# Optimization experiments

Measured on AMD Instinct MI355X. Metric: run time of the kernel, lower is better.

## Reference

```python
import jax, jax.numpy as jnp
import numpy as np
from jax import lax

D_MODEL = 1024
STATE_DIM = 512
BATCH = 4
SEQ_LEN = 8192


def _cayley_eigenvalues(a_params, n):
    # a_full = [0, a_1..a_half, -a_half-1..., antisymmetric tail]
    half = n // 2
    a_full = jnp.zeros((n,), dtype=a_params.dtype)
    a_full = a_full.at[1:half + 1].set(a_params)
    a_full = a_full.at[half + 1:].set(-a_params[::-1][: n - half - 1])
    a_hat = jnp.fft.fft(a_full)            # complex64
    omega = jnp.imag(a_hat)                # (n,), float32
    ones = jnp.ones_like(omega)
    num = lax.complex(ones, -omega)
    den = lax.complex(ones, omega)
    return num / den                        # (n,), |lambda|=1


def setup_inputs() -> dict:
    key = jax.random.key(0)
    k1, k2, k3, k4 = jax.random.split(key, 4)
    u = jax.random.normal(k1, (BATCH, SEQ_LEN, D_MODEL), dtype=jnp.float32)
    a_params = jax.random.normal(k2, (STATE_DIM // 2,), dtype=jnp.float32) * 0.1
    # torch Linear weights: B.weight (state_dim, d_model), C.weight (d_model, state_dim)
    B_w = jax.random.normal(k3, (STATE_DIM, D_MODEL), dtype=jnp.float32) / np.sqrt(D_MODEL)
    C_w = jax.random.normal(k4, (D_MODEL, STATE_DIM), dtype=jnp.float32) / np.sqrt(STATE_DIM)
    D = jnp.ones((D_MODEL,), dtype=jnp.float32)
    return {"u": u, "a_params": a_params, "B_w": B_w, "C_w": C_w, "D": D}


def reference(u, a_params, B_w, C_w, D):
    batch, seq_len, d = u.shape
    n = B_w.shape[0]
    # 1) input projection: (b, t, n)
    Bu = jnp.einsum("btd,nd->btn", u, B_w)
    # 2) per-channel geometric kernel k_j[t] = lambda_j^t
    eig = _cayley_eigenvalues(a_params, n)                 # (n,) complex64
    t = jnp.arange(seq_len, dtype=jnp.float32)
    kernel = jnp.exp(t[:, None] * jnp.log(eig)[None, :])   # (T, n) complex64
    # 3) causal convolution via FFT with next-pow2(2T) padding
    fft_len = 1
    while fft_len < 2 * seq_len:
        fft_len *= 2
    pad = fft_len - seq_len
    kernel_padded = jnp.pad(kernel, ((0, pad), (0, 0)))
    K_hat = jnp.fft.fft(kernel_padded, axis=0)             # (F, n)
    Bu_padded = jnp.pad(Bu, ((0, 0), (0, pad), (0, 0))).astype(jnp.complex64)
    Bu_hat = jnp.fft.fft(Bu_padded, axis=1)                # (b, F, n)
    h = jnp.fft.ifft(K_hat[None] * Bu_hat, axis=1).real[:, :seq_len, :]
    # 4) output projection + skip
    y = jnp.einsum("btn,dn->btd", h, C_w) + D * u
    return y
```

## Files before the change

### kernel.cpp

```cpp
#include <hip/hip_runtime.h>
#include <cstdint>
#include <cstddef>

#define D_MODEL   1024
#define STATE_DIM 512
#define BATCH     4
#define SEQ_LEN   8192
#define M_TOTAL   (BATCH * SEQ_LEN)

typedef unsigned short ushort_t;
typedef __attribute__((ext_vector_type(8))) __bf16 bf16x8;
typedef __attribute__((ext_vector_type(4))) float  f32x4;


__device__ inline ushort_t f2bf(float f) {
  union { float f; uint32_t u; } v; v.f = f;
  uint32_t u = v.u;
  uint32_t r = (u + 0x7FFFu + ((u >> 16) & 1u)) >> 16;
  return (ushort_t)r;
}

__device__ inline void llds16(const void* g, void* l) {
  __builtin_amdgcn_global_load_lds(
      (__attribute__((address_space(1))) void*)(void*)g,
      (__attribute__((address_space(3))) void*)l,
      16, 0, 0);
}


__global__ void convert_f32_bf16(const float* __restrict__ in,
                                 ushort_t* __restrict__ out, int n4) {
  int i = blockIdx.x * blockDim.x + threadIdx.x;
  if (i >= n4) return;
  const float4 v = ((const float4*)in)[i];
  ushort4 o;
  o.x = f2bf(v.x); o.y = f2bf(v.y); o.z = f2bf(v.z); o.w = f2bf(v.w);
  ((ushort4*)out)[i] = o;
}


__global__ void eigen_kernel(const float* __restrict__ a_params,
                             float* __restrict__ lam) {
  __shared__ float af[STATE_DIM];
  const int k = threadIdx.x;
  float v = 0.f;
  if (k >= 1 && k <= STATE_DIM / 2)      v = a_params[k - 1];
  else if (k > STATE_DIM / 2)            v = -a_params[STATE_DIM - k];
  af[k] = v;
  __syncthreads();
  float om = 0.f;
  const float c = 6.283185307179586f / 512.0f;
  for (int n = 1; n < STATE_DIM; ++n) {
    int p = (k * n) & 511;
    om -= af[n] * sinf(c * (float)p);
  }
  const float d  = 1.f / (1.f + om * om);
  const float lr = (1.f - om * om) * d;
  const float li = -2.f * om * d;
  double th = atan2((double)li, (double)lr) * 128.0;
  lam[k]        = lr;
  lam[512 + k]  = li;
  lam[1024 + k] = (float)cos(th);
  lam[1536 + k] = (float)sin(th);
}


template <int KDIM, int NDIM, bool FUSE_SKIP>
__global__ __launch_bounds__(256, 2)
void gemm_bt(const ushort_t* __restrict__ A,
             const ushort_t* __restrict__ Bw,
             float* __restrict__ out,
             const float* __restrict__ skip_u,
             const float* __restrict__ Dvec) {
  __shared__ __align__(16) ushort_t smA[128 * 32];
  __shared__ __align__(16) ushort_t smB[128 * 32];
  const int tid    = threadIdx.x;
  const int wave   = tid >> 6, lane = tid & 63;
  const int lane16 = lane & 15, quad = lane >> 4;
  const int wm = (wave & 1) * 64, wn = (wave >> 1) * 64;
  const int row0 = blockIdx.x * 128;
  const int col0 = blockIdx.y * 128;

  f32x4 acc[4][4];
#pragma unroll
  for (int i = 0; i < 4; ++i)
#pragma unroll
    for (int j = 0; j < 4; ++j) {
      f32x4 z = {0.f, 0.f, 0.f, 0.f};
      acc[i][j] = z;
    }

  for (int k0 = 0; k0 < KDIM; k0 += 32) {
#pragma unroll
    for (int s = 0; s < 2; ++s) {
      const int c = s * 256 + tid;
      const ushort_t* gA = A  + (size_t)(row0 + (c >> 2)) * KDIM + k0 + (c & 3) * 8;
      const ushort_t* gB = Bw + (size_t)(col0 + (c >> 2)) * KDIM + k0 + (c & 3) * 8;
      const int ldsoff = (s * 256 + wave * 64) * 16;
      llds16(gA, (char*)smA + ldsoff);
      llds16(gB, (char*)smB + ldsoff);
    }
    __syncthreads();

    bf16x8 af[4], bfr[4];
#pragma unroll
    for (int mi = 0; mi < 4; ++mi)
      af[mi] = *(const bf16x8*)(smA + (wm + mi * 16 + lane16) * 32 + quad * 8);
#pragma unroll
    for (int ni = 0; ni < 4; ++ni)
      bfr[ni] = *(const bf16x8*)(smB + (wn + ni * 16 + lane16) * 32 + quad * 8);
#pragma unroll
    for (int mi = 0; mi < 4; ++mi)
#pragma unroll
      for (int ni = 0; ni < 4; ++ni)
        acc[mi][ni] = __builtin_amdgcn_mfma_f32_16x16x32_bf16(
            af[mi], bfr[ni], acc[mi][ni], 0, 0, 0);
    __syncthreads();
  }

#pragma unroll
  for (int mi = 0; mi < 4; ++mi) {
#pragma unroll
    for (int ni = 0; ni < 4; ++ni) {
      const int row = row0 + wm + mi * 16 + quad * 4;
      const int col = col0 + wn + ni * 16 + lane16;
      float dv = 0.f;
      if (FUSE_SKIP) dv = Dvec[col];
#pragma unroll
      for (int r = 0; r < 4; ++r) {
        const size_t o = (size_t)(row + r) * NDIM + col;
        float val = acc[mi][ni][r];
        if (FUSE_SKIP) val = fmaf(dv, skip_u[o], val);
        out[o] = val;
      }
    }
  }
}


#define NCHUNK 64
#define CLEN   128
#define SOFF   (BATCH * NCHUNK * STATE_DIM)

__global__ __launch_bounds__(512)
void scan_chunks(const float* __restrict__ Bu, const float* __restrict__ lam,
                 float* __restrict__ S) {
  const int j = threadIdx.x;
  const int c = blockIdx.x & (NCHUNK - 1);
  const int b = blockIdx.x >> 6;
  const float lr = lam[j], li = lam[512 + j];
  const float* p = Bu + ((size_t)(b * SEQ_LEN + c * CLEN)) * STATE_DIM + j;
  float hr = 0.f, hi = 0.f;
#pragma unroll 4
  for (int t = 0; t < CLEN; ++t) {
    const float x  = p[(size_t)t * STATE_DIM];
    const float nr = fmaf(lr, hr, fmaf(-li, hi, x));
    const float ni = fmaf(lr, hi, li * hr);
    hr = nr; hi = ni;
  }
  const size_t o = (size_t)(b * NCHUNK + c) * STATE_DIM + j;
  S[o] = hr; S[SOFF + o] = hi;
}

__global__ __launch_bounds__(512)
void scan_carry(const float* __restrict__ lam, const float* __restrict__ S,
                float* __restrict__ Hin) {
  const int idx = blockIdx.x * blockDim.x + threadIdx.x;
  const int j = idx & 511, b = idx >> 9;
  const float pr = lam[1024 + j], pi = lam[1536 + j];
  float cr = 0.f, ci = 0.f;
  for (int c = 0; c < NCHUNK; ++c) {
    const size_t o = (size_t)(b * NCHUNK + c) * STATE_DIM + j;
    Hin[o] = cr; Hin[SOFF + o] = ci;
    const float sr = S[o], si = S[SOFF + o];
    const float nr = fmaf(pr, cr, fmaf(-pi, ci, sr));
    const float ni = fmaf(pr, ci, fmaf(pi, cr, si));
    cr = nr; ci = ni;
  }
}

__global__ __launch_bounds__(512)
void scan_final(const float* __restrict__ Bu, const float* __restrict__ lam,
                const float* __restrict__ Hin, ushort_t* __restrict__ h) {
  const int j = threadIdx.x;
  const int c = blockIdx.x & (NCHUNK - 1);
  const int b = blockIdx.x >> 6;
  const float lr = lam[j], li = lam[512 + j];
  const size_t so = (size_t)(b * NCHUNK + c) * STATE_DIM + j;
  float hr = Hin[so], hi = Hin[SOFF + so];
  const size_t base = ((size_t)(b * SEQ_LEN + c * CLEN)) * STATE_DIM + j;
#pragma unroll 4
  for (int t = 0; t < CLEN; ++t) {
    const float x  = Bu[base + (size_t)t * STATE_DIM];
    const float nr = fmaf(lr, hr, fmaf(-li, hi, x));
    const float ni = fmaf(lr, hi, li * hr);
    hr = nr; hi = ni;
    h[base + (size_t)t * STATE_DIM] = f2bf(hr);
  }
}


extern "C" void kernel_launch(void* const* d_in, const int* in_sizes, int n_in,
                              void* d_out, int out_size, void* d_ws, size_t ws_size,
                              hipStream_t stream) {
  const float* u  = (const float*)d_in[0];
  const float* ap = (const float*)d_in[1];
  const float* Bw = (const float*)d_in[2];
  const float* Cw = (const float*)d_in[3];
  const float* Dv = (const float*)d_in[4];
  float* y = (float*)d_out;

  char* ws = (char*)d_ws;
  ushort_t* ub  = (ushort_t*)(ws + 0);
  ushort_t* bwb = (ushort_t*)(ws + 67108864);
  ushort_t* cwb = (ushort_t*)(ws + 68157440);
  float*    lam = (float*)   (ws + 69206016);
  float*    Bu  = (float*)   (ws + 69214208);
  ushort_t* hb  = (ushort_t*)(ws + 136323072);
  float*    S   = (float*)   (ws + 169877504);
  float*    Hin = (float*)   (ws + 170926080);

  convert_f32_bf16<<<32768, 256, 0, stream>>>(u,  ub,  (M_TOTAL * D_MODEL) / 4);
  convert_f32_bf16<<<512,   256, 0, stream>>>(Bw, bwb, (STATE_DIM * D_MODEL) / 4);
  convert_f32_bf16<<<512,   256, 0, stream>>>(Cw, cwb, (D_MODEL * STATE_DIM) / 4);
  eigen_kernel<<<1, 512, 0, stream>>>(ap, lam);

  gemm_bt<D_MODEL, STATE_DIM, false>
      <<<dim3(M_TOTAL / 128, STATE_DIM / 128), 256, 0, stream>>>(
          ub, bwb, Bu, nullptr, nullptr);

  scan_chunks<<<BATCH * NCHUNK, 512, 0, stream>>>(Bu, lam, S);
  scan_carry<<<BATCH, 512, 0, stream>>>(lam, S, Hin);
  scan_final<<<BATCH * NCHUNK, 512, 0, stream>>>(Bu, lam, Hin, hb);

  gemm_bt<STATE_DIM, D_MODEL, true>
      <<<dim3(M_TOTAL / 128, D_MODEL / 128), 256, 0, stream>>>(
          hb, cwb, y, u, Dv);
}
```

Measured before the change: 465.7 us.

## Store Bu in bf16, swizzle GEMM LDS, parallelize eigen kernel, bf16 skip

```diff
diff --git a/kernel.cpp b/kernel.cpp
--- a/kernel.cpp
+++ b/kernel.cpp
@@ -18,6 +18,11 @@
   uint32_t u = v.u;
   uint32_t r = (u + 0x7FFFu + ((u >> 16) & 1u)) >> 16;
   return (ushort_t)r;
+}
+
+__device__ inline float bf2f(ushort_t b) {
+  union { uint32_t u; float f; } v; v.u = ((uint32_t)b) << 16;
+  return v.f;
 }
 
 __device__ inline void llds16(const void* g, void* l) {
@@ -39,38 +44,42 @@
 }
 
 
-__global__ void eigen_kernel(const float* __restrict__ a_params,
-                             float* __restrict__ lam) {
-  __shared__ float af[STATE_DIM];
-  const int k = threadIdx.x;
-  float v = 0.f;
-  if (k >= 1 && k <= STATE_DIM / 2)      v = a_params[k - 1];
-  else if (k > STATE_DIM / 2)            v = -a_params[STATE_DIM - k];
-  af[k] = v;
-  __syncthreads();
+__global__ __launch_bounds__(64)
+void eigen_kernel(const float* __restrict__ a_params, float* __restrict__ lam) {
+  const int k = blockIdx.x;
+  const int l = threadIdx.x;
+  const float c = 6.283185307179586f / 512.0f;
   float om = 0.f;
-  const float c = 6.283185307179586f / 512.0f;
-  for (int n = 1; n < STATE_DIM; ++n) {
-    int p = (k * n) & 511;
-    om -= af[n] * sinf(c * (float)p);
-  }
-  const float d  = 1.f / (1.f + om * om);
-  const float lr = (1.f - om * om) * d;
-  const float li = -2.f * om * d;
-  double th = atan2((double)li, (double)lr) * 128.0;
-  lam[k]        = lr;
-  lam[512 + k]  = li;
-  lam[1024 + k] = (float)cos(th);
-  lam[1536 + k] = (float)sin(th);
-}
-
-
-template <int KDIM, int NDIM, bool FUSE_SKIP>
-__global__ __launch_bounds__(256, 2)
+#pragma unroll
+  for (int s = 0; s < 8; ++s) {
+    const int n = s * 64 + l;
+    float v = 0.f;
+    if (n >= 1 && n <= STATE_DIM / 2)      v = a_params[n - 1];
+    else if (n > STATE_DIM / 2)            v = -a_params[STATE_DIM - n];
+    const int p = (k * n) & 511;
+    om -= v * sinf(c * (float)p);
+  }
+#pragma unroll
+  for (int off = 32; off; off >>= 1) om += __shfl_down(om, off);
+  if (l == 0) {
+    const float d  = 1.f / (1.f + om * om);
+    const float lr = (1.f - om * om) * d;
+    const float li = -2.f * om * d;
+    double th = atan2((double)li, (double)lr) * 128.0;
+    lam[k]        = lr;
+    lam[512 + k]  = li;
+    lam[1024 + k] = (float)cos(th);
+    lam[1536 + k] = (float)sin(th);
+  }
+}
+
+
+template <int KDIM, int NDIM, bool OUT_BF16, bool FUSE_SKIP>
+__global__ __launch_bounds__(256, 4)
 void gemm_bt(const ushort_t* __restrict__ A,
              const ushort_t* __restrict__ Bw,
-             float* __restrict__ out,
-             const float* __restrict__ skip_u,
+             void* __restrict__ outv,
+             const ushort_t* __restrict__ skip_b,
              const float* __restrict__ Dvec) {
   __shared__ __align__(16) ushort_t smA[128 * 32];
   __shared__ __align__(16) ushort_t smB[128 * 32];
@@ -90,25 +99,39 @@
       acc[i][j] = z;
     }
 
+  const int s_r0 = tid >> 2;
+  const int s_c0 = (tid & 3) ^ ((s_r0 >> 1) & 3);
+  const int s_r1 = (256 + tid) >> 2;
+  const int s_c1 = (tid & 3) ^ ((s_r1 >> 1) & 3);
+
   for (int k0 = 0; k0 < KDIM; k0 += 32) {
-#pragma unroll
-    for (int s = 0; s < 2; ++s) {
-      const int c = s * 256 + tid;
-      const ushort_t* gA = A  + (size_t)(row0 + (c >> 2)) * KDIM + k0 + (c & 3) * 8;
-      const ushort_t* gB = Bw + (size_t)(col0 + (c >> 2)) * KDIM + k0 + (c & 3) * 8;
-      const int ldsoff = (s * 256 + wave * 64) * 16;
-      llds16(gA, (char*)smA + ldsoff);
-      llds16(gB, (char*)smB + ldsoff);
+    {
+      const ushort_t* gA0 = A  + (size_t)(row0 + s_r0) * KDIM + k0 + s_c0 * 8;
+      const ushort_t* gB0 = Bw + (size_t)(col0 + s_r0) * KDIM + k0 + s_c0 * 8;
+      const ushort_t* gA1 = A  + (size_t)(row0 + s_r1) * KDIM + k0 + s_c1 * 8;
+      const ushort_t* gB1 = Bw + (size_t)(col0 + s_r1) * KDIM + k0 + s_c1 * 8;
+      const int o0 = (wave * 64) * 16;
+      const int o1 = (256 + wave * 64) * 16;
+      llds16(gA0, (char*)smA + o0);
+      llds16(gB0, (char*)smB + o0);
+      llds16(gA1, (char*)smA + o1);
+      llds16(gB1, (char*)smB + o1);
     }
     __syncthreads();
 
     bf16x8 af[4], bfr[4];
 #pragma unroll
-    for (int mi = 0; mi < 4; ++mi)
-      af[mi] = *(const bf16x8*)(smA + (wm + mi * 16 + lane16) * 32 + quad * 8);
-#pragma unroll
-    for (int ni = 0; ni < 4; ++ni)
-      bfr[ni] = *(const bf16x8*)(smB + (wn + ni * 16 + lane16) * 32 + quad * 8);
+    for (int mi = 0; mi < 4; ++mi) {
+      const int m = wm + mi * 16 + lane16;
+      const int pc = quad ^ ((m >> 1) & 3);
+      af[mi] = *(const bf16x8*)(smA + (m * 4 + pc) * 8);
+    }
+#pragma unroll
+    for (int ni = 0; ni < 4; ++ni) {
+      const int n = wn + ni * 16 + lane16;
+      const int pc = quad ^ ((n >> 1) & 3);
+      bfr[ni] = *(const bf16x8*)(smB + (n * 4 + pc) * 8);
+    }
 #pragma unroll
     for (int mi = 0; mi < 4; ++mi)
 #pragma unroll
@@ -130,8 +153,9 @@
       for (int r = 0; r < 4; ++r) {
         const size_t o = (size_t)(row + r) * NDIM + col;
         float val = acc[mi][ni][r];
-        if (FUSE_SKIP) val = fmaf(dv, skip_u[o], val);
-        out[o] = val;
+        if (FUSE_SKIP) val = fmaf(dv, bf2f(skip_b[o]), val);
+        if (OUT_BF16) ((ushort_t*)outv)[o] = f2bf(val);
+        else          ((float*)outv)[o] = val;
       }
     }
   }
@@ -143,17 +167,17 @@
 #define SOFF   (BATCH * NCHUNK * STATE_DIM)
 
 __global__ __launch_bounds__(512)
-void scan_chunks(const float* __restrict__ Bu, const float* __restrict__ lam,
+void scan_chunks(const ushort_t* __restrict__ Bu, const float* __restrict__ lam,
                  float* __restrict__ S) {
   const int j = threadIdx.x;
   const int c = blockIdx.x & (NCHUNK - 1);
   const int b = blockIdx.x >> 6;
   const float lr = lam[j], li = lam[512 + j];
-  const float* p = Bu + ((size_t)(b * SEQ_LEN + c * CLEN)) * STATE_DIM + j;
+  const ushort_t* p = Bu + ((size_t)(b * SEQ_LEN + c * CLEN)) * STATE_DIM + j;
   float hr = 0.f, hi = 0.f;
 #pragma unroll 4
   for (int t = 0; t < CLEN; ++t) {
-    const float x  = p[(size_t)t * STATE_DIM];
+    const float x  = bf2f(p[(size_t)t * STATE_DIM]);
     const float nr = fmaf(lr, hr, fmaf(-li, hi, x));
     const float ni = fmaf(lr, hi, li * hr);
     hr = nr; hi = ni;
@@ -180,7 +204,7 @@
 }
 
 __global__ __launch_bounds__(512)
-void scan_final(const float* __restrict__ Bu, const float* __restrict__ lam,
+void scan_final(const ushort_t* __restrict__ Bu, const float* __restrict__ lam,
                 const float* __restrict__ Hin, ushort_t* __restrict__ h) {
   const int j = threadIdx.x;
   const int c = blockIdx.x & (NCHUNK - 1);
@@ -191,7 +215,7 @@
   const size_t base = ((size_t)(b * SEQ_LEN + c * CLEN)) * STATE_DIM + j;
 #pragma unroll 4
   for (int t = 0; t < CLEN; ++t) {
-    const float x  = Bu[base + (size_t)t * STATE_DIM];
+    const float x  = bf2f(Bu[base + (size_t)t * STATE_DIM]);
     const float nr = fmaf(lr, hr, fmaf(-li, hi, x));
     const float ni = fmaf(lr, hi, li * hr);
     hr = nr; hi = ni;
@@ -215,17 +239,17 @@
   ushort_t* bwb = (ushort_t*)(ws + 67108864);
   ushort_t* cwb = (ushort_t*)(ws + 68157440);
   float*    lam = (float*)   (ws + 69206016);
-  float*    Bu  = (float*)   (ws + 69214208);
-  ushort_t* hb  = (ushort_t*)(ws + 136323072);
-  float*    S   = (float*)   (ws + 169877504);
-  float*    Hin = (float*)   (ws + 170926080);
+  ushort_t* Bu  = (ushort_t*)(ws + 69214208);
+  ushort_t* hb  = (ushort_t*)(ws + 102768640);
+  float*    S   = (float*)   (ws + 136323072);
+  float*    Hin = (float*)   (ws + 137371648);
 
   convert_f32_bf16<<<32768, 256, 0, stream>>>(u,  ub,  (M_TOTAL * D_MODEL) / 4);
   convert_f32_bf16<<<512,   256, 0, stream>>>(Bw, bwb, (STATE_DIM * D_MODEL) / 4);
   convert_f32_bf16<<<512,   256, 0, stream>>>(Cw, cwb, (D_MODEL * STATE_DIM) / 4);
-  eigen_kernel<<<1, 512, 0, stream>>>(ap, lam);
-
-  gemm_bt<D_MODEL, STATE_DIM, false>
+  eigen_kernel<<<512, 64, 0, stream>>>(ap, lam);
+
+  gemm_bt<D_MODEL, STATE_DIM, true, false>
       <<<dim3(M_TOTAL / 128, STATE_DIM / 128), 256, 0, stream>>>(
           ub, bwb, Bu, nullptr, nullptr);
 
@@ -233,7 +257,7 @@
   scan_carry<<<BATCH, 512, 0, stream>>>(lam, S, Hin);
   scan_final<<<BATCH * NCHUNK, 512, 0, stream>>>(Bu, lam, Hin, hb);
 
-  gemm_bt<STATE_DIM, D_MODEL, true>
+  gemm_bt<STATE_DIM, D_MODEL, false, true>
       <<<dim3(M_TOTAL / 128, D_MODEL / 128), 256, 0, stream>>>(
-          hb, cwb, y, u, Dv);
-}
+          hb, cwb, y, ub, Dv);
+}
```

Measured after the change: 392.5 us. 15.7% less time.
